# Performance work log

Hardware: AMD Instinct MI355X
Metric: run time of the kernel (lower is better)

The kernel has to match this reference:

```python
import jax, jax.numpy as jnp
import numpy as np

NUM_HEADS = 12


def setup_inputs() -> dict:
    key = jax.random.key(0)
    ks = jax.random.split(key, 6)
    C = 768
    hd = C // NUM_HEADS  # 64
    H = W = 32
    x = jax.random.normal(ks[0], (4, H, W, C), dtype=jnp.float32)
    # Linear weights stored as (in, out) so y = x @ W (+ b)
    Wqkv = jax.random.normal(ks[1], (C, 3 * C), dtype=jnp.float32) * 0.02
    Wproj = jax.random.normal(ks[2], (C, C), dtype=jnp.float32) * 0.02
    bproj = jax.random.normal(ks[3], (C,), dtype=jnp.float32) * 0.02
    rel_pos_h = jax.random.normal(ks[4], (2 * H - 1, hd), dtype=jnp.float32) * 0.02
    rel_pos_w = jax.random.normal(ks[5], (2 * W - 1, hd), dtype=jnp.float32) * 0.02
    return {"x": x, "Wqkv": Wqkv, "Wproj": Wproj, "bproj": bproj,
            "rel_pos_h": rel_pos_h, "rel_pos_w": rel_pos_w}


def _get_rel_pos(size: int, rel_pos: jnp.ndarray) -> jnp.ndarray:
    # q_size == k_size == size; table already has 2*size-1 entries -> no interpolation
    coords = jnp.arange(size)[:, None] - jnp.arange(size)[None, :] + (size - 1)
    return rel_pos[coords]  # (size, size, head_dim)


def reference(x, Wqkv, Wproj, bproj, rel_pos_h, rel_pos_w):
    B, H, W, C = x.shape
    hn = NUM_HEADS
    hd = C // hn
    scale = hd ** (-0.5)
    S = H * W

    qkv = x @ Wqkv                                   # (B,H,W,3C)
    qkv = qkv.reshape(B, S, 3, hn, hd)
    qkv = jnp.transpose(qkv, (2, 0, 3, 1, 4)).reshape(3, B * hn, S, hd)
    q, k, v = qkv[0], qkv[1], qkv[2]                 # each (B*hn, S, hd)

    # decomposed relative position bias
    Rh = _get_rel_pos(H, rel_pos_h)                  # (H,H,hd)
    Rw = _get_rel_pos(W, rel_pos_w)                  # (W,W,hd)
    r_q = q.reshape(B * hn, H, W, hd)
    rel_h = jnp.einsum('bhwc,hkc->bhwk', r_q, Rh)    # (B*hn,H,W,H)
    rel_w = jnp.einsum('bhwc,wkc->bhwk', r_q, Rw)    # (B*hn,H,W,W)
    bias = rel_h[..., :, None] + rel_w[..., None, :] # (B*hn,H,W,H,W)
    bias = bias.reshape(B * hn, S, S)

    scores = scale * jnp.einsum('bqc,bkc->bqk', q, k) + bias
    attn = jax.nn.softmax(scores, axis=-1)
    out = jnp.einsum('bqk,bkc->bqc', attn, v)        # (B*hn,S,hd)

    out = out.reshape(B, hn, H, W, hd)
    out = jnp.transpose(out, (0, 2, 3, 1, 4)).reshape(B, H, W, C)
    return out @ Wproj + bproj
```

## Files before the change

kernel.cpp:

```cpp
#include <hip/hip_runtime.h>
#include <stddef.h>

typedef __bf16 bf16x8 __attribute__((ext_vector_type(8)));
typedef __bf16 bf16x4 __attribute__((ext_vector_type(4)));
typedef float  f32x4  __attribute__((ext_vector_type(4)));

#define MFMA16(a, b, c) __builtin_amdgcn_mfma_f32_16x16x32_bf16((a), (b), (c), 0, 0, 0)

__device__ __forceinline__ void gload_lds16(const void* gsrc, void* ldst) {
    __builtin_amdgcn_global_load_lds(
        (__attribute__((address_space(1))) void*)gsrc,
        (__attribute__((address_space(3))) void*)ldst,
        16, 0, 0);
}

__global__ void prep_kernel(const float* __restrict__ x, __bf16* __restrict__ xbf,
                            const float* __restrict__ Wqkv, __bf16* __restrict__ WqkvT,
                            const float* __restrict__ Wproj, __bf16* __restrict__ WprojT) {
    __shared__ float tile[32][33];
    const int bx = blockIdx.x, tid = threadIdx.x;
    if (bx < 3072) {
        int i = bx * 256 + tid;
        float4 v = ((const float4*)x)[i];
        bf16x4 o = {(__bf16)v.x, (__bf16)v.y, (__bf16)v.z, (__bf16)v.w};
        ((bf16x4*)xbf)[i] = o;
        return;
    }
    const float* in; __bf16* out; int R, C, c0, r0;
    if (bx < 4800) { int bb = bx - 3072; in = Wqkv;  out = WqkvT;  R = 768; C = 2304;
                     c0 = (bb % 72) * 32; r0 = (bb / 72) * 32; }
    else           { int bb = bx - 4800; in = Wproj; out = WprojT; R = 768; C = 768;
                     c0 = (bb % 24) * 32; r0 = (bb / 24) * 32; }
    const int tx = tid & 31, ty = tid >> 5;
#pragma unroll
    for (int i = 0; i < 32; i += 8)
        tile[ty + i][tx] = in[(size_t)(r0 + ty + i) * C + c0 + tx];
    __syncthreads();
#pragma unroll
    for (int i = 0; i < 32; i += 8)
        out[(size_t)(c0 + ty + i) * R + r0 + tx] = (__bf16)tile[tx][ty + i];
}

__device__ __forceinline__ void gemm_core_bk64(
    const __bf16* __restrict__ A, const __bf16* __restrict__ Bt, int K,
    int m0, int n0, __bf16* aT, __bf16* bT, f32x4 acc[4][4]) {
    const int tid  = threadIdx.x;
    const int wid  = tid >> 6, lane = tid & 63;
    const int quad = lane >> 4, l16 = lane & 15;
    const int wm = (wid >> 1) * 64, wn = (wid & 1) * 64;
    const int r_in = lane >> 3;
    const int cswz = ((lane & 7) ^ r_in) * 8;
    const __bf16* gA = A  + (size_t)(m0 + wid * 8 + r_in) * K + cswz;
    const __bf16* gB = Bt + (size_t)(n0 + wid * 8 + r_in) * K + cswz;
    const int sA = (l16 & 7);
    for (int k0 = 0; k0 < K; k0 += 64) {
        __syncthreads();
#pragma unroll
        for (int j = 0; j < 4; j++) {
            gload_lds16(gA + (size_t)(j * 32) * K + k0, aT + (j * 32 + wid * 8) * 64);
            gload_lds16(gB + (size_t)(j * 32) * K + k0, bT + (j * 32 + wid * 8) * 64);
        }
        __syncthreads();
#pragma unroll
        for (int kh = 0; kh < 2; kh++) {
            bf16x8 af[4], bfr[4];
#pragma unroll
            for (int t = 0; t < 4; t++) {
                const int slot = ((kh * 4 + quad) ^ sA) << 3;
                af[t]  = *(const bf16x8*)(aT + (wm + t * 16 + l16) * 64 + slot);
                bfr[t] = *(const bf16x8*)(bT + (wn + t * 16 + l16) * 64 + slot);
            }
#pragma unroll
            for (int rt = 0; rt < 4; rt++)
#pragma unroll
                for (int ct = 0; ct < 4; ct++)
                    acc[rt][ct] = MFMA16(af[rt], bfr[ct], acc[rt][ct]);
        }
    }
}

__global__ __launch_bounds__(256, 3)
void gemm_qkv_kernel(const __bf16* __restrict__ A, const __bf16* __restrict__ Bt,
                     __bf16* __restrict__ qb, __bf16* __restrict__ kb,
                     __bf16* __restrict__ vtb) {
    __shared__ __bf16 aT[8192], bT[8192];
    f32x4 acc[4][4];
#pragma unroll
    for (int i = 0; i < 4; i++)
#pragma unroll
        for (int j = 0; j < 4; j++) { f32x4 z = {0.f, 0.f, 0.f, 0.f}; acc[i][j] = z; }
    const int m0 = blockIdx.x * 128, n0 = blockIdx.y * 128;
    gemm_core_bk64(A, Bt, 768, m0, n0, aT, bT, acc);
    const int tid = threadIdx.x, wid = tid >> 6, lane = tid & 63;
    const int quad = lane >> 4, l16 = lane & 15;
    const int wm = (wid >> 1) * 64, wn = (wid & 1) * 64;
#pragma unroll
    for (int rt = 0; rt < 4; rt++)
#pragma unroll
        for (int ct = 0; ct < 4; ct++) {
            const int ng = n0 + wn + ct * 16 + l16;
            const int which = ng / 768;
            const int rem = ng - which * 768;
            const int hh = rem >> 6, d = rem & 63;
#pragma unroll
            for (int r = 0; r < 4; r++) {
                const int mg = m0 + wm + rt * 16 + quad * 4 + r;
                const int b = mg >> 10, s = mg & 1023;
                const int bh = b * 12 + hh;
                __bf16 bv = (__bf16)acc[rt][ct][r];
                if (which == 0)      qb[((size_t)bh * 1024 + s) * 64 + d] = bv;
                else if (which == 1) kb[((size_t)bh * 1024 + s) * 64 + d] = bv;
                else                 vtb[((size_t)bh * 64 + d) * 1024 + s] = bv;
            }
        }
}

__global__ __launch_bounds__(256, 3)
void gemm_proj_kernel(const __bf16* __restrict__ A, const __bf16* __restrict__ Bt,
                      const float* __restrict__ bias, float* __restrict__ out) {
    __shared__ __bf16 aT[8192], bT[8192];
    f32x4 acc[4][4];
#pragma unroll
    for (int i = 0; i < 4; i++)
#pragma unroll
        for (int j = 0; j < 4; j++) { f32x4 z = {0.f, 0.f, 0.f, 0.f}; acc[i][j] = z; }
    const int m0 = blockIdx.x * 128, n0 = blockIdx.y * 128;
    gemm_core_bk64(A, Bt, 768, m0, n0, aT, bT, acc);
    const int tid = threadIdx.x, wid = tid >> 6, lane = tid & 63;
    const int quad = lane >> 4, l16 = lane & 15;
    const int wm = (wid >> 1) * 64, wn = (wid & 1) * 64;
#pragma unroll
    for (int rt = 0; rt < 4; rt++)
#pragma unroll
        for (int ct = 0; ct < 4; ct++) {
            const int ng = n0 + wn + ct * 16 + l16;
            const float bb = bias[ng];
#pragma unroll
            for (int r = 0; r < 4; r++) {
                const int mg = m0 + wm + rt * 16 + quad * 4 + r;
                out[(size_t)mg * 768 + ng] = acc[rt][ct][r] + bb;
            }
        }
}

__global__ __launch_bounds__(256, 3)
void attn_kernel(const __bf16* __restrict__ q, const __bf16* __restrict__ kk,
                 const __bf16* __restrict__ vt, const float* __restrict__ rph,
                 const float* __restrict__ rpw, __bf16* __restrict__ aout) {
    __shared__ __bf16 kv[2][8192];
    __shared__ __bf16 pbuf[4][16 * 72];
    __shared__ float  relh[64][33];
    const int tid = threadIdx.x, wid = tid >> 6, lane = tid & 63;
    const int quad = lane >> 4, l16 = lane & 15;
    const int bh = blockIdx.x, qt = blockIdx.y;
    const int b = bh / 12, hh = bh - b * 12;
    const int q0 = qt * 64;
    const int w0 = wid * 16;
    const int h = qt * 2 + (wid >> 1);

    const __bf16* qp = q + ((size_t)bh * 1024 + q0 + w0 + l16) * 64;
    bf16x8 aq0 = *(const bf16x8*)(qp + quad * 8);
    bf16x8 aq1 = *(const bf16x8*)(qp + 32 + quad * 8);

    float* Dw = ((float*)kv) + wid * 1024;
#pragma unroll
    for (int ct = 0; ct < 4; ct++) {
        int j = ct * 16 + l16; if (j > 62) j = 62;
        const float* tb = rpw + (size_t)j * 64;
        float4 t0 = *(const float4*)(tb + quad * 8);
        float4 t1 = *(const float4*)(tb + quad * 8 + 4);
        float4 t2 = *(const float4*)(tb + 32 + quad * 8);
        float4 t3 = *(const float4*)(tb + 32 + quad * 8 + 4);
        bf16x8 b0 = {(__bf16)t0.x, (__bf16)t0.y, (__bf16)t0.z, (__bf16)t0.w,
                     (__bf16)t1.x, (__bf16)t1.y, (__bf16)t1.z, (__bf16)t1.w};
        bf16x8 b1 = {(__bf16)t2.x, (__bf16)t2.y, (__bf16)t2.z, (__bf16)t2.w,
                     (__bf16)t3.x, (__bf16)t3.y, (__bf16)t3.z, (__bf16)t3.w};
        f32x4 z = {0.f, 0.f, 0.f, 0.f};
        z = MFMA16(aq0, b0, z);
        z = MFMA16(aq1, b1, z);
#pragma unroll
        for (int i = 0; i < 4; i++)
            Dw[(quad * 4 + i) * 64 + ct * 16 + l16] = z[i];
    }
#pragma unroll
    for (int ct = 0; ct < 2; ct++) {
        const int tr = h - (ct * 16 + l16) + 31;
        const float* tb = rph + (size_t)tr * 64;
        float4 t0 = *(const float4*)(tb + quad * 8);
        float4 t1 = *(const float4*)(tb + quad * 8 + 4);
        float4 t2 = *(const float4*)(tb + 32 + quad * 8);
        float4 t3 = *(const float4*)(tb + 32 + quad * 8 + 4);
        bf16x8 b0 = {(__bf16)t0.x, (__bf16)t0.y, (__bf16)t0.z, (__bf16)t0.w,
                     (__bf16)t1.x, (__bf16)t1.y, (__bf16)t1.z, (__bf16)t1.w};
        bf16x8 b1 = {(__bf16)t2.x, (__bf16)t2.y, (__bf16)t2.z, (__bf16)t2.w,
                     (__bf16)t3.x, (__bf16)t3.y, (__bf16)t3.z, (__bf16)t3.w};
        f32x4 z = {0.f, 0.f, 0.f, 0.f};
        z = MFMA16(aq0, b0, z);
        z = MFMA16(aq1, b1, z);
#pragma unroll
        for (int i = 0; i < 4; i++)
            relh[w0 + quad * 4 + i][ct * 16 + l16] = z[i];
    }
    float bw[2][4];
#pragma unroll
    for (int r = 0; r < 4; r++) {
        const int rl = quad * 4 + r;
        const int w = (wid & 1) * 16 + rl;
        bw[0][r] = Dw[rl * 64 + w - l16 + 31];
        bw[1][r] = Dw[rl * 64 + w + 15 - l16];
    }
    __syncthreads();

    float l_run[4];
    f32x4 o_acc[4];
#pragma unroll
    for (int r = 0; r < 4; r++) l_run[r] = 0.f;
#pragma unroll
    for (int t = 0; t < 4; t++) { f32x4 z = {0.f, 0.f, 0.f, 0.f}; o_acc[t] = z; }

    const __bf16* kg0 = kk + (size_t)bh * 65536;
    const __bf16* vg0 = vt + (size_t)bh * 65536;
    const int cbase = wid * 2;
    const int srow = lane >> 3;
    const int scol = ((lane & 7) ^ srow) * 8;
    const int swz0 = ((quad ^ (l16 & 7)) << 3);
    const int swz1 = (((quad | 4) ^ (l16 & 7)) << 3);
    __bf16* pw = pbuf[wid];

    auto stage = [&](int buf, int kt) {
        const __bf16* kg = kg0 + kt * 4096;
        const __bf16* vg = vg0 + kt * 64;
        __bf16* kb_ = &kv[buf][0];
        __bf16* vb_ = &kv[buf][4096];
#pragma unroll
        for (int j = 0; j < 2; j++) {
            const int c = cbase + j;
            gload_lds16(kg + (c * 8 + srow) * 64 + scol, kb_ + c * 512);
            gload_lds16(vg + (size_t)(c * 8 + srow) * 1024 + scol, vb_ + c * 512);
        }
    };

    stage(0, 0);
    for (int kt = 0; kt < 16; kt++) {
        const int cur = kt & 1;
        __syncthreads();
        if (kt < 15) stage(1 - cur, kt + 1);
        const __bf16* kbuf = &kv[cur][0];
        const __bf16* vbuf = &kv[cur][4096];

        bf16x8 bk[4][2];
#pragma unroll
        for (int ct = 0; ct < 4; ct++) {
            const int key = ct * 16 + l16;
            bk[ct][0] = *(const bf16x8*)(kbuf + key * 64 + swz0);
            bk[ct][1] = *(const bf16x8*)(kbuf + key * 64 + swz1);
        }

        f32x4 sacc[4];
#pragma unroll
        for (int ct = 0; ct < 4; ct++) {
            f32x4 z = {0.f, 0.f, 0.f, 0.f};
            z = MFMA16(aq0, bk[ct][0], z);
            z = MFMA16(aq1, bk[ct][1], z);
            sacc[ct] = z;
        }
        float bh0[4], bh1[4];
#pragma unroll
        for (int r = 0; r < 4; r++) {
            bh0[r] = relh[w0 + quad * 4 + r][kt * 2];
            bh1[r] = relh[w0 + quad * 4 + r][kt * 2 + 1];
        }
#pragma unroll
        for (int ct = 0; ct < 4; ct++)
#pragma unroll
            for (int r = 0; r < 4; r++) {
                float sv = fmaf(sacc[ct][r], 0.125f,
                                (ct < 2 ? bh0[r] : bh1[r]) + ((ct & 1) ? bw[1][r] : bw[0][r]));
                float p = __expf(sv);
                l_run[r] += p;
                pw[(quad * 4 + r) * 72 + ct * 16 + l16] = (__bf16)p;
            }

        bf16x8 ap0 = *(const bf16x8*)(pw + l16 * 72 + quad * 8);
        bf16x8 ap1 = *(const bf16x8*)(pw + l16 * 72 + 32 + quad * 8);
#pragma unroll
        for (int nt = 0; nt < 4; nt++) {
            const int d = nt * 16 + l16;
            bf16x8 bv0 = *(const bf16x8*)(vbuf + d * 64 + swz0);
            bf16x8 bv1 = *(const bf16x8*)(vbuf + d * 64 + swz1);
            o_acc[nt] = MFMA16(ap0, bv0, o_acc[nt]);
            o_acc[nt] = MFMA16(ap1, bv1, o_acc[nt]);
        }
    }

#pragma unroll
    for (int r = 0; r < 4; r++) {
        float s = l_run[r];
        s += __shfl_xor(s, 1);
        s += __shfl_xor(s, 2);
        s += __shfl_xor(s, 4);
        s += __shfl_xor(s, 8);
        l_run[r] = 1.f / s;
    }
    const int srow_o = q0 + w0 + quad * 4;
#pragma unroll
    for (int nt = 0; nt < 4; nt++)
#pragma unroll
        for (int r = 0; r < 4; r++) {
            float v = o_acc[nt][r] * l_run[r];
            aout[((size_t)b * 1024 + srow_o + r) * 768 + hh * 64 + nt * 16 + l16] = (__bf16)v;
        }
}

extern "C" void kernel_launch(void* const* d_in, const int* in_sizes, int n_in,
                              void* d_out, int out_size, void* d_ws, size_t ws_size,
                              hipStream_t stream) {
    const float* x     = (const float*)d_in[0];
    const float* Wqkv  = (const float*)d_in[1];
    const float* Wproj = (const float*)d_in[2];
    const float* bproj = (const float*)d_in[3];
    const float* rph   = (const float*)d_in[4];
    const float* rpw   = (const float*)d_in[5];
    float* out = (float*)d_out;
    char* ws = (char*)d_ws;

    __bf16* xbf    = (__bf16*)(ws);
    __bf16* WqkvT  = (__bf16*)(ws + 6291456);
    __bf16* WprojT = (__bf16*)(ws + 9830400);
    __bf16* qb     = (__bf16*)(ws + 11010048);
    __bf16* kb     = (__bf16*)(ws + 17301504);
    __bf16* vtb    = (__bf16*)(ws + 23592960);
    __bf16* aob    = (__bf16*)(ws + 29884416);

    prep_kernel<<<dim3(5376), dim3(256), 0, stream>>>(x, xbf, Wqkv, WqkvT, Wproj, WprojT);
    gemm_qkv_kernel<<<dim3(32, 18), dim3(256), 0, stream>>>(xbf, WqkvT, qb, kb, vtb);
    attn_kernel<<<dim3(48, 16), dim3(256), 0, stream>>>(qb, kb, vtb, rph, rpw, aob);
    gemm_proj_kernel<<<dim3(32, 6), dim3(256), 0, stream>>>(aob, WprojT, bproj, out);
}
```

Baseline: 155.1 us.

## Compute transposed S tile so P feeds PV MFMA from registers, V in fp16

The attention kernel now computes S^T (K as the A operand, Q as B), so each lane holds a full query row's probabilities in registers. These are converted to fp16 and fed directly into 16x16x16 f16 MFMAs against V, removing the per-wave LDS round trip for P. V is now stored as fp16 and read straight from global memory into registers instead of being staged through LDS, halving LDS staging. Softmax row sums reduce across quads with two shuffles, and output is written as vector bf16x4. The trade-off is uncoalesced-ish global V loads each tile without LDS reuse across waves, plus a change of V's precision from bf16 to fp16.

```diff
diff --git a/kernel.cpp b/kernel.cpp
--- a/kernel.cpp
+++ b/kernel.cpp
@@ -3,9 +3,11 @@
 
 typedef __bf16 bf16x8 __attribute__((ext_vector_type(8)));
 typedef __bf16 bf16x4 __attribute__((ext_vector_type(4)));
+typedef _Float16 f16x4 __attribute__((ext_vector_type(4)));
 typedef float  f32x4  __attribute__((ext_vector_type(4)));
 
 #define MFMA16(a, b, c) __builtin_amdgcn_mfma_f32_16x16x32_bf16((a), (b), (c), 0, 0, 0)
+#define MFMA16H(a, b, c) __builtin_amdgcn_mfma_f32_16x16x16f16((a), (b), (c), 0, 0, 0)
 
 __device__ __forceinline__ void gload_lds16(const void* gsrc, void* ldst) {
     __builtin_amdgcn_global_load_lds(
@@ -82,7 +84,7 @@
 __global__ __launch_bounds__(256, 3)
 void gemm_qkv_kernel(const __bf16* __restrict__ A, const __bf16* __restrict__ Bt,
                      __bf16* __restrict__ qb, __bf16* __restrict__ kb,
-                     __bf16* __restrict__ vtb) {
+                     _Float16* __restrict__ vtb) {
     __shared__ __bf16 aT[8192], bT[8192];
     f32x4 acc[4][4];
 #pragma unroll
@@ -107,10 +109,9 @@
                 const int mg = m0 + wm + rt * 16 + quad * 4 + r;
                 const int b = mg >> 10, s = mg & 1023;
                 const int bh = b * 12 + hh;
-                __bf16 bv = (__bf16)acc[rt][ct][r];
-                if (which == 0)      qb[((size_t)bh * 1024 + s) * 64 + d] = bv;
-                else if (which == 1) kb[((size_t)bh * 1024 + s) * 64 + d] = bv;
-                else                 vtb[((size_t)bh * 64 + d) * 1024 + s] = bv;
+                if (which == 0)      qb[((size_t)bh * 1024 + s) * 64 + d] = (__bf16)acc[rt][ct][r];
+                else if (which == 1) kb[((size_t)bh * 1024 + s) * 64 + d] = (__bf16)acc[rt][ct][r];
+                else                 vtb[((size_t)bh * 64 + d) * 1024 + s] = (_Float16)acc[rt][ct][r];
             }
         }
 }
@@ -145,10 +146,9 @@
 
 __global__ __launch_bounds__(256, 3)
 void attn_kernel(const __bf16* __restrict__ q, const __bf16* __restrict__ kk,
-                 const __bf16* __restrict__ vt, const float* __restrict__ rph,
+                 const _Float16* __restrict__ vt, const float* __restrict__ rph,
                  const float* __restrict__ rpw, __bf16* __restrict__ aout) {
-    __shared__ __bf16 kv[2][8192];
-    __shared__ __bf16 pbuf[4][16 * 72];
+    __shared__ __bf16 kbuf2[2][4096];
     __shared__ float  relh[64][33];
     const int tid = threadIdx.x, wid = tid >> 6, lane = tid & 63;
     const int quad = lane >> 4, l16 = lane & 15;
@@ -162,7 +162,7 @@
     bf16x8 aq0 = *(const bf16x8*)(qp + quad * 8);
     bf16x8 aq1 = *(const bf16x8*)(qp + 32 + quad * 8);
 
-    float* Dw = ((float*)kv) + wid * 1024;
+    float* Dw = ((float*)kbuf2) + wid * 1024;
 #pragma unroll
     for (int ct = 0; ct < 4; ct++) {
         int j = ct * 16 + l16; if (j > 62) j = 62;
@@ -201,115 +201,99 @@
         for (int i = 0; i < 4; i++)
             relh[w0 + quad * 4 + i][ct * 16 + l16] = z[i];
     }
+    const int wq = (wid & 1) * 16 + l16;
     float bw[2][4];
 #pragma unroll
-    for (int r = 0; r < 4; r++) {
-        const int rl = quad * 4 + r;
-        const int w = (wid & 1) * 16 + rl;
-        bw[0][r] = Dw[rl * 64 + w - l16 + 31];
-        bw[1][r] = Dw[rl * 64 + w + 15 - l16];
-    }
+    for (int hf = 0; hf < 2; hf++)
+#pragma unroll
+        for (int r = 0; r < 4; r++)
+            bw[hf][r] = Dw[l16 * 64 + wq + 31 - hf * 16 - quad * 4 - r];
     __syncthreads();
 
-    float l_run[4];
+    float l_run = 0.f;
     f32x4 o_acc[4];
 #pragma unroll
-    for (int r = 0; r < 4; r++) l_run[r] = 0.f;
-#pragma unroll
     for (int t = 0; t < 4; t++) { f32x4 z = {0.f, 0.f, 0.f, 0.f}; o_acc[t] = z; }
 
-    const __bf16* kg0 = kk + (size_t)bh * 65536;
-    const __bf16* vg0 = vt + (size_t)bh * 65536;
+    const __bf16*   kg0 = kk + (size_t)bh * 65536;
+    const _Float16* vg0 = vt + (size_t)bh * 65536 + (size_t)l16 * 1024 + quad * 4;
     const int cbase = wid * 2;
     const int srow = lane >> 3;
     const int scol = ((lane & 7) ^ srow) * 8;
     const int swz0 = ((quad ^ (l16 & 7)) << 3);
     const int swz1 = (((quad | 4) ^ (l16 & 7)) << 3);
-    __bf16* pw = pbuf[wid];
-
-    auto stage = [&](int buf, int kt) {
+
+    auto stageK = [&](int buf, int kt) {
         const __bf16* kg = kg0 + kt * 4096;
-        const __bf16* vg = vg0 + kt * 64;
-        __bf16* kb_ = &kv[buf][0];
-        __bf16* vb_ = &kv[buf][4096];
+        __bf16* kb_ = &kbuf2[buf][0];
 #pragma unroll
         for (int j = 0; j < 2; j++) {
             const int c = cbase + j;
             gload_lds16(kg + (c * 8 + srow) * 64 + scol, kb_ + c * 512);
-            gload_lds16(vg + (size_t)(c * 8 + srow) * 1024 + scol, vb_ + c * 512);
         }
     };
 
-    stage(0, 0);
+    stageK(0, 0);
     for (int kt = 0; kt < 16; kt++) {
         const int cur = kt & 1;
         __syncthreads();
-        if (kt < 15) stage(1 - cur, kt + 1);
-        const __bf16* kbuf = &kv[cur][0];
-        const __bf16* vbuf = &kv[cur][4096];
-
-        bf16x8 bk[4][2];
+        if (kt < 15) stageK(1 - cur, kt + 1);
+        const __bf16* kbuf = &kbuf2[cur][0];
+
+        f16x4 vf[4][4];
+#pragma unroll
+        for (int dt = 0; dt < 4; dt++) {
+            const _Float16* vp = vg0 + (size_t)dt * 16384 + kt * 64;
+#pragma unroll
+            for (int ct = 0; ct < 4; ct++)
+                vf[dt][ct] = *(const f16x4*)(vp + ct * 16);
+        }
+
+        f32x4 sacc[4];
 #pragma unroll
         for (int ct = 0; ct < 4; ct++) {
             const int key = ct * 16 + l16;
-            bk[ct][0] = *(const bf16x8*)(kbuf + key * 64 + swz0);
-            bk[ct][1] = *(const bf16x8*)(kbuf + key * 64 + swz1);
-        }
-
-        f32x4 sacc[4];
+            bf16x8 bk0 = *(const bf16x8*)(kbuf + key * 64 + swz0);
+            bf16x8 bk1 = *(const bf16x8*)(kbuf + key * 64 + swz1);
+            f32x4 z = {0.f, 0.f, 0.f, 0.f};
+            z = MFMA16(bk0, aq0, z);
+            z = MFMA16(bk1, aq1, z);
+            sacc[ct] = z;
+        }
+
+        const float bh0 = relh[w0 + l16][kt * 2];
+        const float bh1 = relh[w0 + l16][kt * 2 + 1];
+        f16x4 pf[4];
 #pragma unroll
         for (int ct = 0; ct < 4; ct++) {
-            f32x4 z = {0.f, 0.f, 0.f, 0.f};
-            z = MFMA16(aq0, bk[ct][0], z);
-            z = MFMA16(aq1, bk[ct][1], z);
-            sacc[ct] = z;
-        }
-        float bh0[4], bh1[4];
-#pragma unroll
-        for (int r = 0; r < 4; r++) {
-            bh0[r] = relh[w0 + quad * 4 + r][kt * 2];
-            bh1[r] = relh[w0 + quad * 4 + r][kt * 2 + 1];
-        }
-#pragma unroll
-        for (int ct = 0; ct < 4; ct++)
+            const float bhc = (ct < 2) ? bh0 : bh1;
 #pragma unroll
             for (int r = 0; r < 4; r++) {
-                float sv = fmaf(sacc[ct][r], 0.125f,
-                                (ct < 2 ? bh0[r] : bh1[r]) + ((ct & 1) ? bw[1][r] : bw[0][r]));
+                float sv = fmaf(sacc[ct][r], 0.125f, bhc + bw[ct & 1][r]);
                 float p = __expf(sv);
-                l_run[r] += p;
-                pw[(quad * 4 + r) * 72 + ct * 16 + l16] = (__bf16)p;
+                l_run += p;
+                pf[ct][r] = (_Float16)p;
             }
-
-        bf16x8 ap0 = *(const bf16x8*)(pw + l16 * 72 + quad * 8);
-        bf16x8 ap1 = *(const bf16x8*)(pw + l16 * 72 + 32 + quad * 8);
-#pragma unroll
-        for (int nt = 0; nt < 4; nt++) {
-            const int d = nt * 16 + l16;
-            bf16x8 bv0 = *(const bf16x8*)(vbuf + d * 64 + swz0);
-            bf16x8 bv1 = *(const bf16x8*)(vbuf + d * 64 + swz1);
-            o_acc[nt] = MFMA16(ap0, bv0, o_acc[nt]);
-            o_acc[nt] = MFMA16(ap1, bv1, o_acc[nt]);
-        }
-    }
-
-#pragma unroll
-    for (int r = 0; r < 4; r++) {
-        float s = l_run[r];
-        s += __shfl_xor(s, 1);
-        s += __shfl_xor(s, 2);
-        s += __shfl_xor(s, 4);
-        s += __shfl_xor(s, 8);
-        l_run[r] = 1.f / s;
-    }
-    const int srow_o = q0 + w0 + quad * 4;
-#pragma unroll
-    for (int nt = 0; nt < 4; nt++)
-#pragma unroll
-        for (int r = 0; r < 4; r++) {
-            float v = o_acc[nt][r] * l_run[r];
-            aout[((size_t)b * 1024 + srow_o + r) * 768 + hh * 64 + nt * 16 + l16] = (__bf16)v;
-        }
+        }
+
+#pragma unroll
+        for (int dt = 0; dt < 4; dt++)
+#pragma unroll
+            for (int ct = 0; ct < 4; ct++)
+                o_acc[dt] = MFMA16H(vf[dt][ct], pf[ct], o_acc[dt]);
+    }
+
+    l_run += __shfl_xor(l_run, 16);
+    l_run += __shfl_xor(l_run, 32);
+    const float inv = 1.f / l_run;
+    const int srow_o = q0 + w0 + l16;
+    float* obase_chk; (void)obase_chk;
+#pragma unroll
+    for (int dt = 0; dt < 4; dt++) {
+        bf16x4 ov = {(__bf16)(o_acc[dt][0] * inv), (__bf16)(o_acc[dt][1] * inv),
+                     (__bf16)(o_acc[dt][2] * inv), (__bf16)(o_acc[dt][3] * inv)};
+        *(bf16x4*)&aout[((size_t)b * 1024 + srow_o) * 768 + hh * 64 + dt * 16 + quad * 4] = ov;
+    }
 }
 
 extern "C" void kernel_launch(void* const* d_in, const int* in_sizes, int n_in,
@@ -324,13 +308,13 @@
     float* out = (float*)d_out;
     char* ws = (char*)d_ws;
 
-    __bf16* xbf    = (__bf16*)(ws);
-    __bf16* WqkvT  = (__bf16*)(ws + 6291456);
-    __bf16* WprojT = (__bf16*)(ws + 9830400);
-    __bf16* qb     = (__bf16*)(ws + 11010048);
-    __bf16* kb     = (__bf16*)(ws + 17301504);
-    __bf16* vtb    = (__bf16*)(ws + 23592960);
-    __bf16* aob    = (__bf16*)(ws + 29884416);
+    __bf16*   xbf    = (__bf16*)(ws);
+    __bf16*   WqkvT  = (__bf16*)(ws + 6291456);
+    __bf16*   WprojT = (__bf16*)(ws + 9830400);
+    __bf16*   qb     = (__bf16*)(ws + 11010048);
+    __bf16*   kb     = (__bf16*)(ws + 17301504);
+    _Float16* vtb    = (_Float16*)(ws + 23592960);
+    __bf16*   aob    = (__bf16*)(ws + 29884416);
 
     prep_kernel<<<dim3(5376), dim3(256), 0, stream>>>(x, xbf, Wqkv, WqkvT, Wproj, WprojT);
     gemm_qkv_kernel<<<dim3(32, 18), dim3(256), 0, stream>>>(xbf, WqkvT, qb, kb, vtb);
```

Measured after the change: 217.4 us. +40.2%, slower.
